# Performance work log

Hardware: AMD Instinct MI355X
Metric: run time of the kernel (lower is better)

## Reference

```python
import jax, jax.numpy as jnp
import numpy as np

N_NODES = 200_000
N_EDGES = 400_000
EXTRA_NNZ = 3 * N_EDGES
IN_CH = 14
HID = 128
ALPHA = -1.5  # HNHN edge-cardinality exponent
BETA = -0.5   # HNHN node-cardinality exponent


def setup_inputs() -> dict:
    key = jax.random.key(0)
    ks = jax.random.split(key, 16)
    # COO incidence: guarantee every node and every edge has >= 1 entry so
    # cardinality^negative_power stays finite (like real molecular hypergraphs).
    base_rows = jnp.arange(N_NODES, dtype=jnp.int32)
    base_cols = jnp.arange(N_NODES, dtype=jnp.int32) % N_EDGES
    edge_rows = jax.random.randint(ks[0], (N_EDGES,), 0, N_NODES, dtype=jnp.int32)
    edge_cols = jnp.arange(N_EDGES, dtype=jnp.int32)
    rnd_rows = jax.random.randint(ks[1], (EXTRA_NNZ,), 0, N_NODES, dtype=jnp.int32)
    rnd_cols = jax.random.randint(ks[2], (EXTRA_NNZ,), 0, N_EDGES, dtype=jnp.int32)
    inc_rows = jnp.concatenate([base_rows, edge_rows, rnd_rows])
    inc_cols = jnp.concatenate([base_cols, edge_cols, rnd_cols])
    inc_vals = jnp.ones(inc_rows.shape[0], dtype=jnp.float32)

    def glorot(k, shape):
        fan_in, fan_out = shape[0], shape[-1]
        s = jnp.sqrt(2.0 / (fan_in + fan_out)).astype(jnp.float32)
        return jax.random.normal(k, shape, dtype=jnp.float32) * s

    return {
        "x_0": jax.random.normal(ks[3], (N_NODES, IN_CH), dtype=jnp.float32),
        "inc_rows": inc_rows,
        "inc_cols": inc_cols,
        "inc_vals": inc_vals,
        "w0_l1": glorot(ks[4], (IN_CH, HID)),
        "w1_l1": glorot(ks[5], (HID, HID)),
        "b1_l1": glorot(ks[6], (1, HID)),
        "b0_l1": glorot(ks[7], (1, HID)),
        "w0_l2": glorot(ks[8], (HID, HID)),
        "w1_l2": glorot(ks[9], (HID, HID)),
        "b1_l2": glorot(ks[10], (1, HID)),
        "b0_l2": glorot(ks[11], (1, HID)),
        "lin_w": glorot(ks[12], (HID, 1)),
        "lin_b": jnp.zeros((1,), dtype=jnp.float32),
    }


def _normalized_values(inc_rows, inc_cols, inc_vals):
    """HNHN alpha/beta normalization of B (node<-edge) and B^T (edge<-node)."""
    seg = jax.ops.segment_sum
    deg_e = seg(inc_vals, inc_cols, num_segments=N_EDGES)   # |e| per hyperedge
    deg_v = seg(inc_vals, inc_rows, num_segments=N_NODES)   # |v| per node
    e_card = deg_e ** ALPHA
    n_card = deg_v ** BETA
    denom_v = seg(inc_vals * e_card[inc_cols], inc_rows, num_segments=N_NODES)  # (B @ e_card)
    denom_e = seg(inc_vals * n_card[inc_rows], inc_cols, num_segments=N_EDGES)  # (B^T @ n_card)
    # D0_left_alpha^{-1} B D1_right_alpha   and   D1_left_beta^{-1} B^T D0_right_beta
    vals_v_from_e = inc_vals * e_card[inc_cols] / denom_v[inc_rows]
    vals_e_from_v = inc_vals * n_card[inc_rows] / denom_e[inc_cols]
    return vals_v_from_e, vals_e_from_v


def reference(x_0, inc_rows, inc_cols, inc_vals,
              w0_l1, w1_l1, b1_l1, b0_l1,
              w0_l2, w1_l2, b1_l2, b0_l2,
              lin_w, lin_b):
    seg = jax.ops.segment_sum
    vals_v_from_e, vals_e_from_v = _normalized_values(inc_rows, inc_cols, inc_vals)

    def layer(x0, w0, w1, b1, b0):
        # node -> hyperedge: x1 = sigma(Bt_norm @ (x0 W0) + b1)
        m = x0 @ w0                                        # [N_NODES, HID]
        x1 = jax.nn.sigmoid(
            seg(vals_e_from_v[:, None] * m[inc_rows], inc_cols, num_segments=N_EDGES) + b1
        )                                                  # [N_EDGES, HID]
        # hyperedge -> node: x0' = sigma(B_norm @ (x1 W1) + b0)
        m2 = x1 @ w1
        x0n = jax.nn.sigmoid(
            seg(vals_v_from_e[:, None] * m2[inc_cols], inc_rows, num_segments=N_NODES) + b0
        )                                                  # [N_NODES, HID]
        return x0n, x1

    x0, x1 = layer(x_0, w0_l1, w1_l1, b1_l1, b0_l1)
    x0, x1 = layer(x0, w0_l2, w1_l2, b1_l2, b0_l2)
    pooled = jnp.max(x0, axis=0)                           # graph-level max pool [HID]
    return pooled @ lin_w + lin_b                          # [1]
```

## Files before the change

kernel.cpp:

```cpp
#include <hip/hip_runtime.h>
#include <hip/hip_bf16.h>

#define N_NODES 200000
#define N_EDGES 400000
#define HID 128

#define SHIFT 10
#define NB_E 391
#define NB_V 196
#define NBT (NB_E + NB_V)

typedef unsigned int u32;
typedef unsigned short u16;
typedef unsigned char u8;
typedef long long i64;
typedef __attribute__((ext_vector_type(4))) float f32x4;
typedef __attribute__((ext_vector_type(2))) float f32x2;

__device__ inline float sigmoidf(float v) { return 1.0f / (1.0f + __expf(-v)); }

__device__ inline u32 pk4_fp8(float f0, float f1, float f2, float f3) {
  u32 v = __builtin_amdgcn_cvt_pk_fp8_f32(f0, f1, 0, false);
  v = __builtin_amdgcn_cvt_pk_fp8_f32(f2, f3, v, true);
  return v;
}

__device__ inline void acc16_fp8(const uint4& q, float wv, float* a) {
#pragma unroll
  for (int h = 0; h < 4; ++h) {
    u32 u = (&q.x)[h];
    f32x2 p0 = __builtin_amdgcn_cvt_pk_f32_fp8(u, false);
    f32x2 p1 = __builtin_amdgcn_cvt_pk_f32_fp8(u, true);
    a[h * 4 + 0] = fmaf(wv, p0.x, a[h * 4 + 0]);
    a[h * 4 + 1] = fmaf(wv, p0.y, a[h * 4 + 1]);
    a[h * 4 + 2] = fmaf(wv, p1.x, a[h * 4 + 2]);
    a[h * 4 + 3] = fmaf(wv, p1.y, a[h * 4 + 3]);
  }
}


__global__ __launch_bounds__(256) void histA_kernel(
    const int* __restrict__ rows, const int* __restrict__ cols,
    u32* __restrict__ gcnt_e, u32* __restrict__ gcnt_v, int nnz) {
  __shared__ u32 h[NBT];
  const int tid = threadIdx.x;
  for (int j = tid; j < NBT; j += 256) h[j] = 0;
  __syncthreads();
  const int i0 = blockIdx.x * 2048;
#pragma unroll
  for (int k = 0; k < 8; ++k) {
    int i = i0 + k * 256 + tid;
    if (i < nnz) {
      atomicAdd(&h[cols[i] >> SHIFT], 1u);
      atomicAdd(&h[NB_E + (rows[i] >> SHIFT)], 1u);
    }
  }
  __syncthreads();
  for (int j = tid; j < NBT; j += 256) {
    u32 n = h[j];
    if (n) {
      if (j < NB_E) atomicAdd(&gcnt_e[j], n);
      else          atomicAdd(&gcnt_v[j - NB_E], n);
    }
  }
}

__global__ __launch_bounds__(512) void scan_small_kernel(u32* __restrict__ blk, int n) {
  __shared__ u32 tmp[512];
  int t = threadIdx.x;
  u32 v = (t < n) ? blk[t] : 0;
  tmp[t] = v;
  __syncthreads();
  for (int d = 1; d < 512; d <<= 1) {
    u32 x = (t >= d) ? tmp[t - d] : 0;
    __syncthreads();
    tmp[t] += x;
    __syncthreads();
  }
  if (t < n) blk[t] = tmp[t] - v;
}

__global__ void set4_kernel(u32* __restrict__ bbE, u32* __restrict__ bbV,
                            u32* __restrict__ ptr_e, u32* __restrict__ ptr_v,
                            u32 nnz) {
  bbE[NB_E] = nnz;
  bbV[NB_V] = nnz;
  ptr_e[N_EDGES] = nnz;
  ptr_v[N_NODES] = nnz;
}

__global__ __launch_bounds__(256) void bin_kernel(
    const int* __restrict__ rows, const int* __restrict__ cols,
    const float* __restrict__ vals, const u32* __restrict__ bbE,
    const u32* __restrict__ bbV, u32* __restrict__ gcur,
    int2* __restrict__ tmp_e, int2* __restrict__ tmp_v, int nnz) {
  __shared__ u32 h[NBT];
  __shared__ u32 base[NBT];
  __shared__ u32 bb[NBT];
  const int tid = threadIdx.x;
  for (int j = tid; j < NBT; j += 256) {
    h[j] = 0;
    bb[j] = (j < NB_E) ? bbE[j] : bbV[j - NB_E];
  }
  __syncthreads();
  const int i0 = blockIdx.x * 2048;
#pragma unroll
  for (int k = 0; k < 8; ++k) {
    int i = i0 + k * 256 + tid;
    if (i < nnz) {
      atomicAdd(&h[cols[i] >> SHIFT], 1u);
      atomicAdd(&h[NB_E + (rows[i] >> SHIFT)], 1u);
    }
  }
  __syncthreads();
  for (int j = tid; j < NBT; j += 256) {
    u32 n = h[j];
    base[j] = n ? atomicAdd(&gcur[j], n) : 0;
    h[j] = 0;
  }
  __syncthreads();
#pragma unroll
  for (int k = 0; k < 8; ++k) {
    int i = i0 + k * 256 + tid;
    if (i < nnz) {
      int c = cols[i], r = rows[i];
      int vb = __float_as_int(vals[i]);
      int be = c >> SHIFT;
      int bv = NB_E + (r >> SHIFT);
      u32 le = atomicAdd(&h[be], 1u);
      tmp_e[bb[be] + base[be] + le] = make_int2(((c & 1023) << 19) | r, vb);
      u32 lv = atomicAdd(&h[bv], 1u);
      tmp_v[bb[bv] + base[bv] + lv] = make_int2(((r & 1023) << 19) | c, vb);
    }
  }
}

template <bool EDGE>
__global__ __launch_bounds__(512) void build_kernel(
    const int2* __restrict__ tmp, const u32* __restrict__ bukBase,
    u32* __restrict__ ptr, int2* __restrict__ ent, float* __restrict__ card,
    const float* __restrict__ ncard, int S) {
  __shared__ u32 loc[1024];
  __shared__ u32 sstart[1024];
  __shared__ u32 aux[512];
  const int tid = threadIdx.x;
  const int c0 = blockIdx.x << SHIFT;
  const int nseg = min(1024, S - c0);
  const u32 eb = bukBase[blockIdx.x], ee = bukBase[blockIdx.x + 1];
  loc[tid] = 0;
  loc[tid + 512] = 0;
  __syncthreads();
  for (u32 j = eb + tid; j < ee; j += 512)
    atomicAdd(&loc[(u32)tmp[j].x >> 19], 1u);
  __syncthreads();
  u32 a0 = loc[2 * tid], a1 = loc[2 * tid + 1];
  u32 T = a0 + a1;
  aux[tid] = T;
  __syncthreads();
  for (int d = 1; d < 512; d <<= 1) {
    u32 x = (tid >= d) ? aux[tid - d] : 0;
    __syncthreads();
    aux[tid] += x;
    __syncthreads();
  }
  u32 off = aux[tid] - T;
  loc[2 * tid] = off;
  loc[2 * tid + 1] = off + a0;
  sstart[2 * tid] = off;
  sstart[2 * tid + 1] = off + a0;
  __syncthreads();
  for (int k = tid; k < nseg; k += 512) ptr[c0 + k] = eb + loc[k];
  __syncthreads();
  for (u32 j = eb + tid; j < ee; j += 512) {
    int2 e = tmp[j];
    u32 s = (u32)e.x >> 19;
    u32 p = atomicAdd(&loc[s], 1u);
    ent[eb + p] = make_int2(e.x & 0x7FFFF, e.y);
  }
  __syncthreads();
  for (int k = tid; k < nseg; k += 512) {
    u32 s0 = eb + sstart[k], s1 = eb + loc[k];
    float s = 0.f;
    for (u32 j = s0; j < s1; ++j) s += __int_as_float(ent[j].y);
    float t = rsqrtf(s);
    card[c0 + k] = EDGE ? t * t * t : t;
    if (EDGE) {
      float d = 0.f;
      for (u32 j = s0; j < s1; ++j) {
        int2 en = ent[j];
        d += __int_as_float(en.y) * ncard[en.x];
      }
      float inv = 1.f / d;
      for (u32 j = s0; j < s1; ++j) {
        int2 en = ent[j];
        ent[j].y = __float_as_int(__int_as_float(en.y) * ncard[en.x] * inv);
      }
    }
  }
}

__global__ __launch_bounds__(256) void segV_kernel(
    const u32* __restrict__ ptr_v, int2* __restrict__ ent_v,
    const float* __restrict__ e_card) {
  int i = blockIdx.x * 256 + threadIdx.x;
  if (i >= N_NODES) return;
  u32 b = ptr_v[i], e = ptr_v[i + 1];
  float s = 0.f;
  for (u32 j = b; j < e; ++j) {
    int2 en = ent_v[j];
    s += __int_as_float(en.y) * e_card[en.x];
  }
  float inv = 1.f / s;
  for (u32 j = b; j < e; ++j) {
    int2 en = ent_v[j];
    ent_v[j].y = __float_as_int(__int_as_float(en.y) * e_card[en.x] * inv);
  }
}


__global__ __launch_bounds__(256) void mm14n_kernel(
    const float* __restrict__ x0, const float* __restrict__ w,
    u8* __restrict__ U, int N) {
  __shared__ float ws[14 * HID];
  const int tid = threadIdx.x;
  for (int i = tid; i < 14 * HID; i += 256) ws[i] = w[i];
  __syncthreads();
  const int row = blockIdx.x * 8 + (tid >> 5);
  const int c4 = (tid & 31) << 2;
  if (row >= N) return;
  const float* xr = x0 + (size_t)row * 14;
  float a0 = 0.f, a1 = 0.f, a2 = 0.f, a3 = 0.f;
#pragma unroll
  for (int k = 0; k < 14; ++k) {
    const float xv = xr[k];
    const float* wr = ws + k * HID + c4;
    a0 = fmaf(xv, wr[0], a0);
    a1 = fmaf(xv, wr[1], a1);
    a2 = fmaf(xv, wr[2], a2);
    a3 = fmaf(xv, wr[3], a3);
  }
  *(u32*)(U + (size_t)row * HID + c4) = pk4_fp8(a0, a1, a2, a3);
}

template <bool SIG, bool POOL>
__global__ __launch_bounds__(256, 1) void im128_mfma_kernel(
    u8* __restrict__ buf, const float* __restrict__ w,
    const float* __restrict__ b, u32* __restrict__ pooled, int R) {
  const int tid = threadIdx.x;
  const int wave = tid >> 6;
  const int lo = tid & 15;
  const int hi = (tid & 63) >> 4;
  i64 wf[8][4];
#pragma unroll
  for (int n = 0; n < 8; ++n)
#pragma unroll
    for (int t = 0; t < 4; ++t) {
      const float* wp = w + (size_t)(t * 32 + hi * 8) * HID + n * 16 + lo;
      u32 w0 = pk4_fp8(wp[0], wp[HID], wp[2 * HID], wp[3 * HID]);
      u32 w1 = pk4_fp8(wp[4 * HID], wp[5 * HID], wp[6 * HID], wp[7 * HID]);
      wf[n][t] = (i64)w0 | ((i64)w1 << 32);
    }
  float bias[8];
  if (SIG) {
#pragma unroll
    for (int n = 0; n < 8; ++n) bias[n] = b[n * 16 + lo];
  }
  float pm[8];
#pragma unroll
  for (int n = 0; n < 8; ++n) pm[n] = 0.f;

  for (int rb = blockIdx.x * 64 + wave * 16; rb < R; rb += gridDim.x * 64) {
    const u8* xp = buf + (size_t)(rb + lo) * HID + hi * 8;
    i64 a0 = *(const i64*)(xp);
    i64 a1 = *(const i64*)(xp + 32);
    i64 a2 = *(const i64*)(xp + 64);
    i64 a3 = *(const i64*)(xp + 96);
    u8* yp = buf + (size_t)(rb + hi * 4) * HID + lo;
#pragma unroll
    for (int n = 0; n < 8; ++n) {
      f32x4 c = {0.f, 0.f, 0.f, 0.f};
      c = __builtin_amdgcn_mfma_f32_16x16x32_fp8_fp8(a0, wf[n][0], c, 0, 0, 0);
      c = __builtin_amdgcn_mfma_f32_16x16x32_fp8_fp8(a1, wf[n][1], c, 0, 0, 0);
      c = __builtin_amdgcn_mfma_f32_16x16x32_fp8_fp8(a2, wf[n][2], c, 0, 0, 0);
      c = __builtin_amdgcn_mfma_f32_16x16x32_fp8_fp8(a3, wf[n][3], c, 0, 0, 0);
#pragma unroll
      for (int r = 0; r < 4; ++r) {
        float v = SIG ? sigmoidf(c[r] + bias[n]) : c[r];
        if (POOL) {
          pm[n] = fmaxf(pm[n], v);
        } else {
          u32 q = __builtin_amdgcn_cvt_pk_fp8_f32(v, v, 0, false);
          yp[(size_t)r * HID + n * 16] = (u8)q;
        }
      }
    }
  }

  if (POOL) {
    __shared__ u32 pmax[HID];
    for (int i = tid; i < HID; i += 256) pmax[i] = 0;
    __syncthreads();
#pragma unroll
    for (int n = 0; n < 8; ++n)
      atomicMax(&pmax[n * 16 + lo], __float_as_uint(pm[n]));
    __syncthreads();
    if (tid < HID) atomicMax(&pooled[tid], pmax[tid]);
  }
}


template <bool SIG>
__global__ __launch_bounds__(256) void gather128_kernel(
    const u32* __restrict__ ptr, const int2* __restrict__ ent,
    const u8* __restrict__ src, const float* __restrict__ b,
    u8* __restrict__ dst, int S) {
  long long t = (long long)blockIdx.x * 256 + threadIdx.x;
  int r = (int)(t >> 3);
  if (r >= S) return;
  const int c16 = (int)(t & 7) << 4;
  u32 beg = ptr[r], end = ptr[r + 1];
  float a[16];
#pragma unroll
  for (int i = 0; i < 16; ++i) a[i] = 0.f;
  u32 j = beg;
  for (; j + 2 <= end; j += 2) {
    int2 e0 = ent[j];
    int2 e1 = ent[j + 1];
    const uint4 q0 = *(const uint4*)(src + (size_t)e0.x * HID + c16);
    const uint4 q1 = *(const uint4*)(src + (size_t)e1.x * HID + c16);
    acc16_fp8(q0, __int_as_float(e0.y), a);
    acc16_fp8(q1, __int_as_float(e1.y), a);
  }
  if (j < end) {
    int2 e0 = ent[j];
    const uint4 q0 = *(const uint4*)(src + (size_t)e0.x * HID + c16);
    acc16_fp8(q0, __int_as_float(e0.y), a);
  }
  if (SIG) {
#pragma unroll
    for (int h = 0; h < 4; ++h) {
      float4 bb = *(const float4*)(b + c16 + h * 4);
      a[h * 4 + 0] = sigmoidf(a[h * 4 + 0] + bb.x);
      a[h * 4 + 1] = sigmoidf(a[h * 4 + 1] + bb.y);
      a[h * 4 + 2] = sigmoidf(a[h * 4 + 2] + bb.z);
      a[h * 4 + 3] = sigmoidf(a[h * 4 + 3] + bb.w);
    }
  }
  uint4 pk;
  pk.x = pk4_fp8(a[0], a[1], a[2], a[3]);
  pk.y = pk4_fp8(a[4], a[5], a[6], a[7]);
  pk.z = pk4_fp8(a[8], a[9], a[10], a[11]);
  pk.w = pk4_fp8(a[12], a[13], a[14], a[15]);
  *(uint4*)(dst + (size_t)r * HID + c16) = pk;
}


__global__ __launch_bounds__(128) void final_kernel(
    const u32* __restrict__ pooled, const float* __restrict__ lin_w,
    const float* __restrict__ lin_b, float* __restrict__ out) {
  __shared__ float red[64];
  int t = threadIdx.x;
  float v = __uint_as_float(pooled[t]) * lin_w[t];
  if (t >= 64) red[t - 64] = v;
  __syncthreads();
  if (t < 64) {
    v += red[t];
#pragma unroll
    for (int off = 32; off > 0; off >>= 1) v += __shfl_down(v, off);
    if (t == 0) out[0] = v + lin_b[0];
  }
}

__global__ void diag_kernel(float* out, float v) { out[0] = v; }


extern "C" void kernel_launch(void* const* d_in, const int* in_sizes, int n_in,
                              void* d_out, int out_size, void* d_ws, size_t ws_size,
                              hipStream_t stream) {
  const float* x0     = (const float*)d_in[0];
  const int*   rows   = (const int*)d_in[1];
  const int*   cols   = (const int*)d_in[2];
  const float* vals   = (const float*)d_in[3];
  const float* w0_l1  = (const float*)d_in[4];
  const float* w1_l1  = (const float*)d_in[5];
  const float* b1_l1  = (const float*)d_in[6];
  const float* b0_l1  = (const float*)d_in[7];
  const float* w0_l2  = (const float*)d_in[8];
  const float* w1_l2  = (const float*)d_in[9];
  const float* b1_l2  = (const float*)d_in[10];
  const float* b0_l2  = (const float*)d_in[11];
  const float* lin_w  = (const float*)d_in[12];
  const float* lin_b  = (const float*)d_in[13];
  float* out = (float*)d_out;
  const int nnz = in_sizes[1];

  char* wsp = (char*)d_ws;
  size_t off = 0;
  auto carve = [&](size_t bytes) -> char* {
    char* p = wsp + off;
    off = (off + bytes + 511) & ~(size_t)511;
    return p;
  };
  float* n_card  = (float*)carve((size_t)N_NODES * 4);
  float* e_card  = (float*)carve((size_t)N_EDGES * 4);
  u32*   ptr_v   = (u32*)carve((size_t)(N_NODES + 1) * 4);
  u32*   ptr_e   = (u32*)carve((size_t)(N_EDGES + 1) * 4);
  u32*   bbE     = (u32*)carve((NB_E + 1) * 4);
  u32*   bbV     = (u32*)carve((NB_V + 1) * 4);
  u32*   gcur    = (u32*)carve(NBT * 4);
  int2*  ent_v   = (int2*)carve((size_t)nnz * 8);
  int2*  ent_e   = (int2*)carve((size_t)nnz * 8);
  u32*   pooled  = (u32*)carve(HID * 4);
  u8*    bufN    = (u8*)carve((size_t)N_NODES * HID);
  u8*    bufE    = (u8*)carve((size_t)N_EDGES * HID);
  int2*  tmp_e   = (int2*)carve((size_t)nnz * 8);
  int2*  tmp_v   = (int2*)carve((size_t)nnz * 8);

  if (off > ws_size) {
    diag_kernel<<<1, 1, 0, stream>>>(out, (float)(ws_size >> 20));
    return;
  }

  hipMemsetAsync(bbE, 0, (NB_E + 1) * 4, stream);
  hipMemsetAsync(bbV, 0, (NB_V + 1) * 4, stream);
  hipMemsetAsync(gcur, 0, NBT * 4, stream);
  hipMemsetAsync(pooled, 0, HID * 4, stream);

  const int nbBin = (nnz + 2047) / 2048;

  histA_kernel<<<nbBin, 256, 0, stream>>>(rows, cols, bbE, bbV, nnz);
  scan_small_kernel<<<1, 512, 0, stream>>>(bbE, NB_E);
  scan_small_kernel<<<1, 512, 0, stream>>>(bbV, NB_V);
  set4_kernel<<<1, 1, 0, stream>>>(bbE, bbV, ptr_e, ptr_v, (u32)nnz);
  bin_kernel<<<nbBin, 256, 0, stream>>>(rows, cols, vals, bbE, bbV, gcur,
                                        tmp_e, tmp_v, nnz);
  build_kernel<false><<<NB_V, 512, 0, stream>>>(tmp_v, bbV, ptr_v, ent_v,
                                                n_card, nullptr, N_NODES);
  build_kernel<true><<<NB_E, 512, 0, stream>>>(tmp_e, bbE, ptr_e, ent_e,
                                               e_card, n_card, N_EDGES);
  segV_kernel<<<(N_NODES + 255) / 256, 256, 0, stream>>>(ptr_v, ent_v, e_card);

  const int nbE8 = (int)(((long long)N_EDGES * 8 + 255) / 256);
  const int nbN8 = (int)(((long long)N_NODES * 8 + 255) / 256);

  mm14n_kernel<<<N_NODES / 8, 256, 0, stream>>>(x0, w0_l1, bufN, N_NODES);
  gather128_kernel<true><<<nbE8, 256, 0, stream>>>(ptr_e, ent_e, bufN,
                                                   b1_l1, bufE, N_EDGES);
  gather128_kernel<false><<<nbN8, 256, 0, stream>>>(ptr_v, ent_v, bufE,
                                                    nullptr, bufN, N_NODES);
  im128_mfma_kernel<true, false><<<1024, 256, 0, stream>>>(bufN, w1_l1, b0_l1,
                                                           nullptr, N_NODES);

  im128_mfma_kernel<false, false><<<1024, 256, 0, stream>>>(bufN, w0_l2, nullptr,
                                                            nullptr, N_NODES);
  gather128_kernel<true><<<nbE8, 256, 0, stream>>>(ptr_e, ent_e, bufN,
                                                   b1_l2, bufE, N_EDGES);
  gather128_kernel<false><<<nbN8, 256, 0, stream>>>(ptr_v, ent_v, bufE,
                                                    nullptr, bufN, N_NODES);
  im128_mfma_kernel<true, true><<<1024, 256, 0, stream>>>(bufN, w1_l2, b0_l2,
                                                          pooled, N_NODES);

  final_kernel<<<1, 128, 0, stream>>>(pooled, lin_w, lin_b, out);
}
```

Baseline: 509.9 us.

## Fuse layer-boundary matmuls, vectorize binning loads, split segV across thread pairs

Merges the two back-to-back 128x128 MFMA passes (sigmoid(x@W1+b) then @W0 of layer two) into one kernel. The intermediate is staged in shared memory and re-quantized to fp8, which saves a full read and write of the node buffer plus one launch. The histogram and binning kernels now load four rows, columns and values per thread as vector loads, using smaller blocks. segV now assigns two threads per node and combines their sums with a shuffle. The fused kernel holds two weight fragment sets in registers, which raises register pressure.

```diff
diff --git a/kernel.cpp b/kernel.cpp
--- a/kernel.cpp
+++ b/kernel.cpp
@@ -4,6 +4,7 @@
 #define N_NODES 200000
 #define N_EDGES 400000
 #define HID 128
+#define LDSW 132
 
 #define SHIFT 10
 #define NB_E 391
@@ -38,7 +39,6 @@
   }
 }
 
-
 __global__ __launch_bounds__(256) void histA_kernel(
     const int* __restrict__ rows, const int* __restrict__ cols,
     u32* __restrict__ gcnt_e, u32* __restrict__ gcnt_v, int nnz) {
@@ -46,15 +46,27 @@
   const int tid = threadIdx.x;
   for (int j = tid; j < NBT; j += 256) h[j] = 0;
   __syncthreads();
-  const int i0 = blockIdx.x * 2048;
-#pragma unroll
-  for (int k = 0; k < 8; ++k) {
-    int i = i0 + k * 256 + tid;
-    if (i < nnz) {
-      atomicAdd(&h[cols[i] >> SHIFT], 1u);
-      atomicAdd(&h[NB_E + (rows[i] >> SHIFT)], 1u);
-    }
-  }
+  const int i0 = blockIdx.x * 1024 + tid * 4;
+  int4 rr, cc;
+  if (i0 + 3 < nnz) {
+    rr = *(const int4*)(rows + i0);
+    cc = *(const int4*)(cols + i0);
+  } else {
+    int* rp = &rr.x; int* cp = &cc.x;
+#pragma unroll
+    for (int k = 0; k < 4; ++k) {
+      int i = i0 + k;
+      rp[k] = (i < nnz) ? rows[i] : 0;
+      cp[k] = (i < nnz) ? cols[i] : 0;
+    }
+  }
+  const int n4 = min(4, nnz - i0);
+#pragma unroll
+  for (int k = 0; k < 4; ++k)
+    if (k < n4) {
+      atomicAdd(&h[(&cc.x)[k] >> SHIFT], 1u);
+      atomicAdd(&h[NB_E + ((&rr.x)[k] >> SHIFT)], 1u);
+    }
   __syncthreads();
   for (int j = tid; j < NBT; j += 256) {
     u32 n = h[j];
@@ -103,15 +115,30 @@
     bb[j] = (j < NB_E) ? bbE[j] : bbV[j - NB_E];
   }
   __syncthreads();
-  const int i0 = blockIdx.x * 2048;
-#pragma unroll
-  for (int k = 0; k < 8; ++k) {
-    int i = i0 + k * 256 + tid;
-    if (i < nnz) {
-      atomicAdd(&h[cols[i] >> SHIFT], 1u);
-      atomicAdd(&h[NB_E + (rows[i] >> SHIFT)], 1u);
-    }
-  }
+  const int i0 = blockIdx.x * 1024 + tid * 4;
+  int4 rr, cc;
+  float4 vv;
+  if (i0 + 3 < nnz) {
+    rr = *(const int4*)(rows + i0);
+    cc = *(const int4*)(cols + i0);
+    vv = *(const float4*)(vals + i0);
+  } else {
+    int* rp = &rr.x; int* cp = &cc.x; float* vp = &vv.x;
+#pragma unroll
+    for (int k = 0; k < 4; ++k) {
+      int i = i0 + k;
+      rp[k] = (i < nnz) ? rows[i] : 0;
+      cp[k] = (i < nnz) ? cols[i] : 0;
+      vp[k] = (i < nnz) ? vals[i] : 0.f;
+    }
+  }
+  const int n4 = min(4, nnz - i0);
+#pragma unroll
+  for (int k = 0; k < 4; ++k)
+    if (k < n4) {
+      atomicAdd(&h[(&cc.x)[k] >> SHIFT], 1u);
+      atomicAdd(&h[NB_E + ((&rr.x)[k] >> SHIFT)], 1u);
+    }
   __syncthreads();
   for (int j = tid; j < NBT; j += 256) {
     u32 n = h[j];
@@ -120,11 +147,10 @@
   }
   __syncthreads();
 #pragma unroll
-  for (int k = 0; k < 8; ++k) {
-    int i = i0 + k * 256 + tid;
-    if (i < nnz) {
-      int c = cols[i], r = rows[i];
-      int vb = __float_as_int(vals[i]);
+  for (int k = 0; k < 4; ++k)
+    if (k < n4) {
+      int c = (&cc.x)[k], r = (&rr.x)[k];
+      int vb = __float_as_int((&vv.x)[k]);
       int be = c >> SHIFT;
       int bv = NB_E + (r >> SHIFT);
       u32 le = atomicAdd(&h[be], 1u);
@@ -132,7 +158,6 @@
       u32 lv = atomicAdd(&h[bv], 1u);
       tmp_v[bb[bv] + base[bv] + lv] = make_int2(((r & 1023) << 19) | c, vb);
     }
-  }
 }
 
 template <bool EDGE>
@@ -202,16 +227,19 @@
 __global__ __launch_bounds__(256) void segV_kernel(
     const u32* __restrict__ ptr_v, int2* __restrict__ ent_v,
     const float* __restrict__ e_card) {
-  int i = blockIdx.x * 256 + threadIdx.x;
+  int t = blockIdx.x * 256 + threadIdx.x;
+  int i = t >> 1;
+  int half = t & 1;
   if (i >= N_NODES) return;
   u32 b = ptr_v[i], e = ptr_v[i + 1];
   float s = 0.f;
-  for (u32 j = b; j < e; ++j) {
+  for (u32 j = b + half; j < e; j += 2) {
     int2 en = ent_v[j];
     s += __int_as_float(en.y) * e_card[en.x];
   }
+  s += __shfl_xor(s, 1);
   float inv = 1.f / s;
-  for (u32 j = b; j < e; ++j) {
+  for (u32 j = b + half; j < e; j += 2) {
     int2 en = ent_v[j];
     ent_v[j].y = __float_as_int(__int_as_float(en.y) * e_card[en.x] * inv);
   }
@@ -240,6 +268,19 @@
     a3 = fmaf(xv, wr[3], a3);
   }
   *(u32*)(U + (size_t)row * HID + c4) = pk4_fp8(a0, a1, a2, a3);
+}
+
+__device__ inline void load_wfrags(const float* __restrict__ w, int lo, int hi,
+                                   i64 wf[8][4]) {
+#pragma unroll
+  for (int n = 0; n < 8; ++n)
+#pragma unroll
+    for (int t = 0; t < 4; ++t) {
+      const float* wp = w + (size_t)(t * 32 + hi * 8) * HID + n * 16 + lo;
+      u32 w0 = pk4_fp8(wp[0], wp[HID], wp[2 * HID], wp[3 * HID]);
+      u32 w1 = pk4_fp8(wp[4 * HID], wp[5 * HID], wp[6 * HID], wp[7 * HID]);
+      wf[n][t] = (i64)w0 | ((i64)w1 << 32);
+    }
 }
 
 template <bool SIG, bool POOL>
@@ -251,15 +292,7 @@
   const int lo = tid & 15;
   const int hi = (tid & 63) >> 4;
   i64 wf[8][4];
-#pragma unroll
-  for (int n = 0; n < 8; ++n)
-#pragma unroll
-    for (int t = 0; t < 4; ++t) {
-      const float* wp = w + (size_t)(t * 32 + hi * 8) * HID + n * 16 + lo;
-      u32 w0 = pk4_fp8(wp[0], wp[HID], wp[2 * HID], wp[3 * HID]);
-      u32 w1 = pk4_fp8(wp[4 * HID], wp[5 * HID], wp[6 * HID], wp[7 * HID]);
-      wf[n][t] = (i64)w0 | ((i64)w1 << 32);
-    }
+  load_wfrags(w, lo, hi, wf);
   float bias[8];
   if (SIG) {
 #pragma unroll
@@ -305,6 +338,66 @@
       atomicMax(&pmax[n * 16 + lo], __float_as_uint(pm[n]));
     __syncthreads();
     if (tid < HID) atomicMax(&pooled[tid], pmax[tid]);
+  }
+}
+
+__global__ __launch_bounds__(256, 1) void im128_dual_kernel(
+    u8* __restrict__ buf, const float* __restrict__ w1,
+    const float* __restrict__ b, const float* __restrict__ w2, int R) {
+  const int tid = threadIdx.x;
+  const int wave = tid >> 6;
+  const int lo = tid & 15;
+  const int hi = (tid & 63) >> 4;
+  i64 wf1[8][4], wf2[8][4];
+  load_wfrags(w1, lo, hi, wf1);
+  load_wfrags(w2, lo, hi, wf2);
+  float bias[8];
+#pragma unroll
+  for (int n = 0; n < 8; ++n) bias[n] = b[n * 16 + lo];
+  __shared__ float xs[4][16 * LDSW];
+  float* xw = xs[wave];
+
+  for (int rb = blockIdx.x * 64 + wave * 16; rb < R; rb += gridDim.x * 64) {
+    const u8* xp = buf + (size_t)(rb + lo) * HID + hi * 8;
+    i64 a0 = *(const i64*)(xp);
+    i64 a1 = *(const i64*)(xp + 32);
+    i64 a2 = *(const i64*)(xp + 64);
+    i64 a3 = *(const i64*)(xp + 96);
+#pragma unroll
+    for (int n = 0; n < 8; ++n) {
+      f32x4 c = {0.f, 0.f, 0.f, 0.f};
+      c = __builtin_amdgcn_mfma_f32_16x16x32_fp8_fp8(a0, wf1[n][0], c, 0, 0, 0);
+      c = __builtin_amdgcn_mfma_f32_16x16x32_fp8_fp8(a1, wf1[n][1], c, 0, 0, 0);
+      c = __builtin_amdgcn_mfma_f32_16x16x32_fp8_fp8(a2, wf1[n][2], c, 0, 0, 0);
+      c = __builtin_amdgcn_mfma_f32_16x16x32_fp8_fp8(a3, wf1[n][3], c, 0, 0, 0);
+#pragma unroll
+      for (int r = 0; r < 4; ++r)
+        xw[(hi * 4 + r) * LDSW + n * 16 + lo] = sigmoidf(c[r] + bias[n]);
+    }
+    i64 A[4];
+#pragma unroll
+    for (int t = 0; t < 4; ++t) {
+      const float* rp = xw + lo * LDSW + t * 32 + hi * 8;
+      float4 f0 = *(const float4*)rp;
+      float4 f1 = *(const float4*)(rp + 4);
+      u32 p0 = pk4_fp8(f0.x, f0.y, f0.z, f0.w);
+      u32 p1 = pk4_fp8(f1.x, f1.y, f1.z, f1.w);
+      A[t] = (i64)p0 | ((i64)p1 << 32);
+    }
+    u8* yp = buf + (size_t)(rb + hi * 4) * HID + lo;
+#pragma unroll
+    for (int n = 0; n < 8; ++n) {
+      f32x4 c = {0.f, 0.f, 0.f, 0.f};
+      c = __builtin_amdgcn_mfma_f32_16x16x32_fp8_fp8(A[0], wf2[n][0], c, 0, 0, 0);
+      c = __builtin_amdgcn_mfma_f32_16x16x32_fp8_fp8(A[1], wf2[n][1], c, 0, 0, 0);
+      c = __builtin_amdgcn_mfma_f32_16x16x32_fp8_fp8(A[2], wf2[n][2], c, 0, 0, 0);
+      c = __builtin_amdgcn_mfma_f32_16x16x32_fp8_fp8(A[3], wf2[n][3], c, 0, 0, 0);
+#pragma unroll
+      for (int r = 0; r < 4; ++r) {
+        u32 q = __builtin_amdgcn_cvt_pk_fp8_f32(c[r], c[r], 0, false);
+        yp[(size_t)r * HID + n * 16] = (u8)q;
+      }
+    }
   }
 }
 
@@ -426,19 +519,19 @@
   hipMemsetAsync(gcur, 0, NBT * 4, stream);
   hipMemsetAsync(pooled, 0, HID * 4, stream);
 
-  const int nbBin = (nnz + 2047) / 2048;
-
-  histA_kernel<<<nbBin, 256, 0, stream>>>(rows, cols, bbE, bbV, nnz);
+  const int nb1024 = (nnz + 1023) / 1024;
+
+  histA_kernel<<<nb1024, 256, 0, stream>>>(rows, cols, bbE, bbV, nnz);
   scan_small_kernel<<<1, 512, 0, stream>>>(bbE, NB_E);
   scan_small_kernel<<<1, 512, 0, stream>>>(bbV, NB_V);
   set4_kernel<<<1, 1, 0, stream>>>(bbE, bbV, ptr_e, ptr_v, (u32)nnz);
-  bin_kernel<<<nbBin, 256, 0, stream>>>(rows, cols, vals, bbE, bbV, gcur,
-                                        tmp_e, tmp_v, nnz);
+  bin_kernel<<<nb1024, 256, 0, stream>>>(rows, cols, vals, bbE, bbV, gcur,
+                                         tmp_e, tmp_v, nnz);
   build_kernel<false><<<NB_V, 512, 0, stream>>>(tmp_v, bbV, ptr_v, ent_v,
                                                 n_card, nullptr, N_NODES);
   build_kernel<true><<<NB_E, 512, 0, stream>>>(tmp_e, bbE, ptr_e, ent_e,
                                                e_card, n_card, N_EDGES);
-  segV_kernel<<<(N_NODES + 255) / 256, 256, 0, stream>>>(ptr_v, ent_v, e_card);
+  segV_kernel<<<(2 * N_NODES + 255) / 256, 256, 0, stream>>>(ptr_v, ent_v, e_card);
 
   const int nbE8 = (int)(((long long)N_EDGES * 8 + 255) / 256);
   const int nbN8 = (int)(((long long)N_NODES * 8 + 255) / 256);
@@ -448,11 +541,8 @@
                                                    b1_l1, bufE, N_EDGES);
   gather128_kernel<false><<<nbN8, 256, 0, stream>>>(ptr_v, ent_v, bufE,
                                                     nullptr, bufN, N_NODES);
-  im128_mfma_kernel<true, false><<<1024, 256, 0, stream>>>(bufN, w1_l1, b0_l1,
-                                                           nullptr, N_NODES);
-
-  im128_mfma_kernel<false, false><<<1024, 256, 0, stream>>>(bufN, w0_l2, nullptr,
-                                                            nullptr, N_NODES);
+  im128_dual_kernel<<<1024, 256, 0, stream>>>(bufN, w1_l1, b0_l1, w0_l2, N_NODES);
+
   gather128_kernel<true><<<nbE8, 256, 0, stream>>>(ptr_e, ent_e, bufN,
                                                    b1_l2, bufE, N_EDGES);
   gather128_kernel<false><<<nbN8, 256, 0, stream>>>(ptr_v, ent_v, bufE,
```

Result: slower. 555.7 us (+9.0%).

## Fuse histogram and binning into one pass using fixed-capacity bucket storage

Applied to the files above, without the earlier changes.

Removes the separate histogram kernel by having the binning kernel write entries into fixed-capacity per-bucket slots and count bucket sizes with global atomics. The bucket counts are scanned afterwards, and the build kernels read each bucket from its fixed slot. The segment-normalization kernel now splits each node's entries across two lanes and combines them with a shuffle. This saves one full read pass over the incidence arrays, but relies on the capacity constants never being exceeded by any bucket, with no overflow check.

```diff
diff --git a/kernel.cpp b/kernel.cpp
--- a/kernel.cpp
+++ b/kernel.cpp
@@ -9,6 +9,8 @@
 #define NB_E 391
 #define NB_V 196
 #define NBT (NB_E + NB_V)
+#define CAP_E 6144
+#define CAP_V 10240
 
 typedef unsigned int u32;
 typedef unsigned short u16;
@@ -38,17 +40,18 @@
   }
 }
 
-
-__global__ __launch_bounds__(256) void histA_kernel(
+__global__ __launch_bounds__(256) void bin_kernel(
     const int* __restrict__ rows, const int* __restrict__ cols,
-    u32* __restrict__ gcnt_e, u32* __restrict__ gcnt_v, int nnz) {
+    const float* __restrict__ vals, u32* __restrict__ bkE,
+    u32* __restrict__ bkV, int2* __restrict__ tmp_e, int2* __restrict__ tmp_v,
+    int nnz) {
   __shared__ u32 h[NBT];
+  __shared__ u32 base[NBT];
   const int tid = threadIdx.x;
   for (int j = tid; j < NBT; j += 256) h[j] = 0;
   __syncthreads();
-  const int i0 = blockIdx.x * 2048;
-#pragma unroll
-  for (int k = 0; k < 8; ++k) {
+  const int i0 = blockIdx.x * 4096;
+  for (int k = 0; k < 16; ++k) {
     int i = i0 + k * 256 + tid;
     if (i < nnz) {
       atomicAdd(&h[cols[i] >> SHIFT], 1u);
@@ -58,69 +61,13 @@
   __syncthreads();
   for (int j = tid; j < NBT; j += 256) {
     u32 n = h[j];
-    if (n) {
-      if (j < NB_E) atomicAdd(&gcnt_e[j], n);
-      else          atomicAdd(&gcnt_v[j - NB_E], n);
-    }
-  }
-}
-
-__global__ __launch_bounds__(512) void scan_small_kernel(u32* __restrict__ blk, int n) {
-  __shared__ u32 tmp[512];
-  int t = threadIdx.x;
-  u32 v = (t < n) ? blk[t] : 0;
-  tmp[t] = v;
-  __syncthreads();
-  for (int d = 1; d < 512; d <<= 1) {
-    u32 x = (t >= d) ? tmp[t - d] : 0;
-    __syncthreads();
-    tmp[t] += x;
-    __syncthreads();
-  }
-  if (t < n) blk[t] = tmp[t] - v;
-}
-
-__global__ void set4_kernel(u32* __restrict__ bbE, u32* __restrict__ bbV,
-                            u32* __restrict__ ptr_e, u32* __restrict__ ptr_v,
-                            u32 nnz) {
-  bbE[NB_E] = nnz;
-  bbV[NB_V] = nnz;
-  ptr_e[N_EDGES] = nnz;
-  ptr_v[N_NODES] = nnz;
-}
-
-__global__ __launch_bounds__(256) void bin_kernel(
-    const int* __restrict__ rows, const int* __restrict__ cols,
-    const float* __restrict__ vals, const u32* __restrict__ bbE,
-    const u32* __restrict__ bbV, u32* __restrict__ gcur,
-    int2* __restrict__ tmp_e, int2* __restrict__ tmp_v, int nnz) {
-  __shared__ u32 h[NBT];
-  __shared__ u32 base[NBT];
-  __shared__ u32 bb[NBT];
-  const int tid = threadIdx.x;
-  for (int j = tid; j < NBT; j += 256) {
+    base[j] = n ? ((j < NB_E) ? atomicAdd(&bkE[j], n)
+                              : atomicAdd(&bkV[j - NB_E], n))
+                : 0;
     h[j] = 0;
-    bb[j] = (j < NB_E) ? bbE[j] : bbV[j - NB_E];
-  }
-  __syncthreads();
-  const int i0 = blockIdx.x * 2048;
-#pragma unroll
-  for (int k = 0; k < 8; ++k) {
-    int i = i0 + k * 256 + tid;
-    if (i < nnz) {
-      atomicAdd(&h[cols[i] >> SHIFT], 1u);
-      atomicAdd(&h[NB_E + (rows[i] >> SHIFT)], 1u);
-    }
-  }
-  __syncthreads();
-  for (int j = tid; j < NBT; j += 256) {
-    u32 n = h[j];
-    base[j] = n ? atomicAdd(&gcur[j], n) : 0;
-    h[j] = 0;
-  }
-  __syncthreads();
-#pragma unroll
-  for (int k = 0; k < 8; ++k) {
+  }
+  __syncthreads();
+  for (int k = 0; k < 16; ++k) {
     int i = i0 + k * 256 + tid;
     if (i < nnz) {
       int c = cols[i], r = rows[i];
@@ -128,16 +75,42 @@
       int be = c >> SHIFT;
       int bv = NB_E + (r >> SHIFT);
       u32 le = atomicAdd(&h[be], 1u);
-      tmp_e[bb[be] + base[be] + le] = make_int2(((c & 1023) << 19) | r, vb);
+      tmp_e[(size_t)be * CAP_E + base[be] + le] =
+          make_int2(((c & 1023) << 19) | r, vb);
       u32 lv = atomicAdd(&h[bv], 1u);
-      tmp_v[bb[bv] + base[bv] + lv] = make_int2(((r & 1023) << 19) | c, vb);
-    }
-  }
+      tmp_v[(size_t)(bv - NB_E) * CAP_V + base[bv] + lv] =
+          make_int2(((r & 1023) << 19) | c, vb);
+    }
+  }
+}
+
+__global__ __launch_bounds__(512) void scan_small_kernel(u32* __restrict__ blk, int n) {
+  __shared__ u32 tmp[512];
+  int t = threadIdx.x;
+  u32 v = (t < n) ? blk[t] : 0;
+  tmp[t] = v;
+  __syncthreads();
+  for (int d = 1; d < 512; d <<= 1) {
+    u32 x = (t >= d) ? tmp[t - d] : 0;
+    __syncthreads();
+    tmp[t] += x;
+    __syncthreads();
+  }
+  if (t < n) blk[t] = tmp[t] - v;
+}
+
+__global__ void set4_kernel(u32* __restrict__ bkE, u32* __restrict__ bkV,
+                            u32* __restrict__ ptr_e, u32* __restrict__ ptr_v,
+                            u32 nnz) {
+  bkE[NB_E] = nnz;
+  bkV[NB_V] = nnz;
+  ptr_e[N_EDGES] = nnz;
+  ptr_v[N_NODES] = nnz;
 }
 
 template <bool EDGE>
 __global__ __launch_bounds__(512) void build_kernel(
-    const int2* __restrict__ tmp, const u32* __restrict__ bukBase,
+    const int2* __restrict__ tmp, int cap, const u32* __restrict__ bukBase,
     u32* __restrict__ ptr, int2* __restrict__ ent, float* __restrict__ card,
     const float* __restrict__ ncard, int S) {
   __shared__ u32 loc[1024];
@@ -147,11 +120,13 @@
   const int c0 = blockIdx.x << SHIFT;
   const int nseg = min(1024, S - c0);
   const u32 eb = bukBase[blockIdx.x], ee = bukBase[blockIdx.x + 1];
+  const u32 cnt = ee - eb;
+  const int2* tp = tmp + (size_t)blockIdx.x * cap;
   loc[tid] = 0;
   loc[tid + 512] = 0;
   __syncthreads();
-  for (u32 j = eb + tid; j < ee; j += 512)
-    atomicAdd(&loc[(u32)tmp[j].x >> 19], 1u);
+  for (u32 j = tid; j < cnt; j += 512)
+    atomicAdd(&loc[(u32)tp[j].x >> 19], 1u);
   __syncthreads();
   u32 a0 = loc[2 * tid], a1 = loc[2 * tid + 1];
   u32 T = a0 + a1;
@@ -171,8 +146,8 @@
   __syncthreads();
   for (int k = tid; k < nseg; k += 512) ptr[c0 + k] = eb + loc[k];
   __syncthreads();
-  for (u32 j = eb + tid; j < ee; j += 512) {
-    int2 e = tmp[j];
+  for (u32 j = tid; j < cnt; j += 512) {
+    int2 e = tp[j];
     u32 s = (u32)e.x >> 19;
     u32 p = atomicAdd(&loc[s], 1u);
     ent[eb + p] = make_int2(e.x & 0x7FFFF, e.y);
@@ -202,16 +177,19 @@
 __global__ __launch_bounds__(256) void segV_kernel(
     const u32* __restrict__ ptr_v, int2* __restrict__ ent_v,
     const float* __restrict__ e_card) {
-  int i = blockIdx.x * 256 + threadIdx.x;
+  int t = blockIdx.x * 256 + threadIdx.x;
+  int i = t >> 1;
+  int half = t & 1;
   if (i >= N_NODES) return;
   u32 b = ptr_v[i], e = ptr_v[i + 1];
   float s = 0.f;
-  for (u32 j = b; j < e; ++j) {
+  for (u32 j = b + half; j < e; j += 2) {
     int2 en = ent_v[j];
     s += __int_as_float(en.y) * e_card[en.x];
   }
+  s += __shfl_xor(s, 1);
   float inv = 1.f / s;
-  for (u32 j = b; j < e; ++j) {
+  for (u32 j = b + half; j < e; j += 2) {
     int2 en = ent_v[j];
     ent_v[j].y = __float_as_int(__int_as_float(en.y) * e_card[en.x] * inv);
   }
@@ -240,6 +218,19 @@
     a3 = fmaf(xv, wr[3], a3);
   }
   *(u32*)(U + (size_t)row * HID + c4) = pk4_fp8(a0, a1, a2, a3);
+}
+
+__device__ inline void load_wfrags(const float* __restrict__ w, int lo, int hi,
+                                   i64 wf[8][4]) {
+#pragma unroll
+  for (int n = 0; n < 8; ++n)
+#pragma unroll
+    for (int t = 0; t < 4; ++t) {
+      const float* wp = w + (size_t)(t * 32 + hi * 8) * HID + n * 16 + lo;
+      u32 w0 = pk4_fp8(wp[0], wp[HID], wp[2 * HID], wp[3 * HID]);
+      u32 w1 = pk4_fp8(wp[4 * HID], wp[5 * HID], wp[6 * HID], wp[7 * HID]);
+      wf[n][t] = (i64)w0 | ((i64)w1 << 32);
+    }
 }
 
 template <bool SIG, bool POOL>
@@ -251,15 +242,7 @@
   const int lo = tid & 15;
   const int hi = (tid & 63) >> 4;
   i64 wf[8][4];
-#pragma unroll
-  for (int n = 0; n < 8; ++n)
-#pragma unroll
-    for (int t = 0; t < 4; ++t) {
-      const float* wp = w + (size_t)(t * 32 + hi * 8) * HID + n * 16 + lo;
-      u32 w0 = pk4_fp8(wp[0], wp[HID], wp[2 * HID], wp[3 * HID]);
-      u32 w1 = pk4_fp8(wp[4 * HID], wp[5 * HID], wp[6 * HID], wp[7 * HID]);
-      wf[n][t] = (i64)w0 | ((i64)w1 << 32);
-    }
+  load_wfrags(w, lo, hi, wf);
   float bias[8];
   if (SIG) {
 #pragma unroll
@@ -405,40 +388,37 @@
   float* e_card  = (float*)carve((size_t)N_EDGES * 4);
   u32*   ptr_v   = (u32*)carve((size_t)(N_NODES + 1) * 4);
   u32*   ptr_e   = (u32*)carve((size_t)(N_EDGES + 1) * 4);
-  u32*   bbE     = (u32*)carve((NB_E + 1) * 4);
-  u32*   bbV     = (u32*)carve((NB_V + 1) * 4);
-  u32*   gcur    = (u32*)carve(NBT * 4);
+  u32*   bkE     = (u32*)carve((NB_E + 1) * 4);
+  u32*   bkV     = (u32*)carve((NB_V + 1) * 4);
   int2*  ent_v   = (int2*)carve((size_t)nnz * 8);
   int2*  ent_e   = (int2*)carve((size_t)nnz * 8);
   u32*   pooled  = (u32*)carve(HID * 4);
   u8*    bufN    = (u8*)carve((size_t)N_NODES * HID);
   u8*    bufE    = (u8*)carve((size_t)N_EDGES * HID);
-  int2*  tmp_e   = (int2*)carve((size_t)nnz * 8);
-  int2*  tmp_v   = (int2*)carve((size_t)nnz * 8);
+  int2*  tmp_e   = (int2*)carve((size_t)NB_E * CAP_E * 8);
+  int2*  tmp_v   = (int2*)carve((size_t)NB_V * CAP_V * 8);
 
   if (off > ws_size) {
     diag_kernel<<<1, 1, 0, stream>>>(out, (float)(ws_size >> 20));
     return;
   }
 
-  hipMemsetAsync(bbE, 0, (NB_E + 1) * 4, stream);
-  hipMemsetAsync(bbV, 0, (NB_V + 1) * 4, stream);
-  hipMemsetAsync(gcur, 0, NBT * 4, stream);
+  hipMemsetAsync(bkE, 0, (NB_E + 1) * 4, stream);
+  hipMemsetAsync(bkV, 0, (NB_V + 1) * 4, stream);
   hipMemsetAsync(pooled, 0, HID * 4, stream);
 
-  const int nbBin = (nnz + 2047) / 2048;
-
-  histA_kernel<<<nbBin, 256, 0, stream>>>(rows, cols, bbE, bbV, nnz);
-  scan_small_kernel<<<1, 512, 0, stream>>>(bbE, NB_E);
-  scan_small_kernel<<<1, 512, 0, stream>>>(bbV, NB_V);
-  set4_kernel<<<1, 1, 0, stream>>>(bbE, bbV, ptr_e, ptr_v, (u32)nnz);
-  bin_kernel<<<nbBin, 256, 0, stream>>>(rows, cols, vals, bbE, bbV, gcur,
+  const int nbBin = (nnz + 4095) / 4096;
+
+  bin_kernel<<<nbBin, 256, 0, stream>>>(rows, cols, vals, bkE, bkV,
                                         tmp_e, tmp_v, nnz);
-  build_kernel<false><<<NB_V, 512, 0, stream>>>(tmp_v, bbV, ptr_v, ent_v,
-                                                n_card, nullptr, N_NODES);
-  build_kernel<true><<<NB_E, 512, 0, stream>>>(tmp_e, bbE, ptr_e, ent_e,
-                                               e_card, n_card, N_EDGES);
-  segV_kernel<<<(N_NODES + 255) / 256, 256, 0, stream>>>(ptr_v, ent_v, e_card);
+  scan_small_kernel<<<1, 512, 0, stream>>>(bkE, NB_E);
+  scan_small_kernel<<<1, 512, 0, stream>>>(bkV, NB_V);
+  set4_kernel<<<1, 1, 0, stream>>>(bkE, bkV, ptr_e, ptr_v, (u32)nnz);
+  build_kernel<false><<<NB_V, 512, 0, stream>>>(tmp_v, CAP_V, bkV, ptr_v,
+                                                ent_v, n_card, nullptr, N_NODES);
+  build_kernel<true><<<NB_E, 512, 0, stream>>>(tmp_e, CAP_E, bkE, ptr_e,
+                                               ent_e, e_card, n_card, N_EDGES);
+  segV_kernel<<<(2 * N_NODES + 255) / 256, 256, 0, stream>>>(ptr_v, ent_v, e_card);
 
   const int nbE8 = (int)(((long long)N_EDGES * 8 + 255) / 256);
   const int nbN8 = (int)(((long long)N_NODES * 8 + 255) / 256);
```

Measured after the change: 471.6 us. 1.08x faster.
